# Kernel optimization log

Hardware: AMD Instinct MI355X
Metric: run time of the kernel (lower is better)

Reference implementation:

```python
import jax, jax.numpy as jnp
import numpy as np

E = 1024
H = 16
D = E // H  # 64
SCALE = float(D ** 0.5)  # module MULTIPLIES by sqrt(d_head), faithful to source


def setup_inputs() -> dict:
    key = jax.random.key(0)
    k1, k2, k3 = jax.random.split(key, 3)
    x = jax.random.normal(k1, (4, 2048, E), dtype=jnp.float32)
    # store weights as [in, out] so forward is x @ W (equiv to torch Linear with W.T)
    w_qkv = jax.random.normal(k2, (E, 3 * E), dtype=jnp.float32) * (1.0 / np.sqrt(E))
    w_out = jax.random.normal(k3, (E, E), dtype=jnp.float32) * (1.0 / np.sqrt(E))
    return {"x": x, "w_qkv": w_qkv, "w_out": w_out}


def reference(x, w_qkv, w_out):
    b, t, _ = x.shape
    qkv = x @ w_qkv  # [b, t, 3E]
    # einops 'b t (d k h) -> k b h t d' with k=3, h=H: innermost axis is h
    qkv = qkv.reshape(b, t, D, 3, H)
    qkv = jnp.transpose(qkv, (3, 0, 4, 1, 2))  # [3, b, h, t, d]
    q, k, v = qkv[0], qkv[1], qkv[2]
    energy = jnp.einsum('bhid,bhjd->bhij', q, k) * SCALE  # note: multiply, per source
    attn = jax.nn.softmax(energy, axis=-1)
    o = jnp.einsum('bhij,bhjd->bhid', attn, v)
    o = jnp.transpose(o, (0, 2, 1, 3)).reshape(b, t, H * D)  # 'b h t d -> b t (h d)'
    return o @ w_out
```

## Files before the change

### kernel.cpp

```cpp
#include <hip/hip_runtime.h>

typedef __attribute__((ext_vector_type(4))) float f32x4;
typedef __attribute__((ext_vector_type(16))) float f32x16;
typedef __attribute__((ext_vector_type(8))) short bf16x8;
typedef __attribute__((ext_vector_type(4))) unsigned short u16x4;

#define NB 4
#define NT 2048
#define NE 1024
#define NH 16
#define ND 64
#define NM (NB*NT)

__device__ inline unsigned short f2bf(float f){
  unsigned int u = __float_as_uint(f);
  return (unsigned short)((u + 0x7fffu + ((u >> 16) & 1u)) >> 16);
}
__device__ inline float bf2f(unsigned short s){
  return __uint_as_float(((unsigned int)s) << 16);
}
__device__ inline unsigned short f2h(float f){
  union { _Float16 h; unsigned short u; } c;
  c.h = (_Float16)f;
  return c.u;
}
__device__ inline float h2f(unsigned short s){
  union { _Float16 h; unsigned short u; } c;
  c.u = s;
  return (float)c.h;
}
__device__ inline f32x4 mfma16b(bf16x8 a, bf16x8 b, f32x4 c){
  return __builtin_amdgcn_mfma_f32_16x16x32_bf16(a, b, c, 0, 0, 0);
}
__device__ inline f32x4 mfma16h(bf16x8 a, bf16x8 b, f32x4 c){
  return __builtin_amdgcn_mfma_f32_16x16x32_f16(a, b, c, 0, 0, 0);
}
__device__ inline f32x16 mfma32h(bf16x8 a, bf16x8 b, f32x16 c){
  return __builtin_amdgcn_mfma_f32_32x32x16_f16(a, b, c, 0, 0, 0);
}
__device__ inline void gload_lds16(const unsigned short* g, unsigned short* l){
  __builtin_amdgcn_global_load_lds(
      (const __attribute__((address_space(1))) void*)g,
      (__attribute__((address_space(3))) void*)l, 16, 0, 0);
}
__device__ inline float max3f(float a, float b, float c){
  float r;
  asm("v_max3_f32 %0, %1, %2, %3" : "=v"(r) : "v"(a), "v"(b), "v"(c));
  return r;
}

__global__ __launch_bounds__(256) void prep_x_k(const float* __restrict__ x,
    unsigned short* __restrict__ xh, int n4){
  int stride = gridDim.x * 256;
  for (int i = blockIdx.x * 256 + threadIdx.x; i < n4; i += stride){
    f32x4 v = ((const f32x4*)x)[i];
    u16x4 o;
    #pragma unroll
    for (int j = 0; j < 4; j++) o[j] = f2h(v[j]);
    ((u16x4*)xh)[i] = o;
  }
}

__global__ __launch_bounds__(256) void prep_wq_k(const float* __restrict__ w,
    unsigned short* __restrict__ wq){
  __shared__ float tile[32][33];
  int tx = threadIdx.x & 31, ty = threadIdx.x >> 5;
  int c0 = blockIdx.x * 32, k0 = blockIdx.y * 32;
  #pragma unroll
  for (int i = 0; i < 32; i += 8)
    tile[ty + i][tx] = w[(size_t)(k0 + ty + i) * 3072 + c0 + tx];
  __syncthreads();
  #pragma unroll
  for (int i = 0; i < 32; i += 8){
    int col = c0 + ty + i;
    int d = col / 48, r = col % 48;
    int kk = r >> 4, h = r & 15;
    int n = kk * 1024 + h * 64 + d;
    wq[(size_t)n * NE + k0 + tx] = f2h(tile[tx][ty + i]);
  }
}

__global__ __launch_bounds__(256) void prep_wo_k(const float* __restrict__ w,
    unsigned short* __restrict__ wt){
  __shared__ float tile[32][33];
  int tx = threadIdx.x & 31, ty = threadIdx.x >> 5;
  int n0 = blockIdx.x * 32, k0 = blockIdx.y * 32;
  #pragma unroll
  for (int i = 0; i < 32; i += 8)
    tile[ty + i][tx] = w[(size_t)(k0 + ty + i) * NE + n0 + tx];
  __syncthreads();
  #pragma unroll
  for (int i = 0; i < 32; i += 8)
    wt[(size_t)(n0 + ty + i) * NE + k0 + tx] = f2bf(tile[tx][ty + i]);
}

template<int EPI>
__global__ __launch_bounds__(256) void gemm_k(
    const unsigned short* __restrict__ A,
    const unsigned short* __restrict__ Bt,
    float* __restrict__ Cf,
    unsigned short* __restrict__ Qh,
    unsigned short* __restrict__ Kh, unsigned short* __restrict__ Kl,
    unsigned short* __restrict__ Vt,
    int M, int N, int K){
  __shared__ unsigned short lds[2][128 * 32];
  const int tid = threadIdx.x;
  const int w = tid >> 6, l = tid & 63;
  const int wr = w >> 1, wc = w & 1;
  const int m0 = blockIdx.y * 128, n0 = blockIdx.x * 128;

  f32x4 acc[4][4];
  #pragma unroll
  for (int i = 0; i < 4; i++)
    #pragma unroll
    for (int j = 0; j < 4; j++) acc[i][j] = (f32x4){0.f, 0.f, 0.f, 0.f};

  const int lr = l >> 2;
  const int lkb = (l & 3) * 8;

  for (int k0 = 0; k0 < K; k0 += 32){
    #pragma unroll
    for (int cc = 0; cc < 2; cc++){
      int c = w + cc * 4;
      gload_lds16(A  + (size_t)(m0 + c * 16 + lr) * K + k0 + lkb, &lds[0][c * 512]);
      gload_lds16(Bt + (size_t)(n0 + c * 16 + lr) * K + k0 + lkb, &lds[1][c * 512]);
    }
    __syncthreads();
    bf16x8 af[4], bfr[4];
    #pragma unroll
    for (int mi = 0; mi < 4; mi++)
      af[mi] = *(bf16x8*)&lds[0][(wr * 64 + mi * 16 + (l & 15)) * 32 + (l >> 4) * 8];
    #pragma unroll
    for (int ni = 0; ni < 4; ni++)
      bfr[ni] = *(bf16x8*)&lds[1][(wc * 64 + ni * 16 + (l & 15)) * 32 + (l >> 4) * 8];
    #pragma unroll
    for (int mi = 0; mi < 4; mi++)
      #pragma unroll
      for (int ni = 0; ni < 4; ni++)
        acc[mi][ni] = EPI ? mfma16h(af[mi], bfr[ni], acc[mi][ni])
                          : mfma16b(af[mi], bfr[ni], acc[mi][ni]);
    __syncthreads();
  }

  #pragma unroll
  for (int mi = 0; mi < 4; mi++){
    #pragma unroll
    for (int ni = 0; ni < 4; ni++){
      #pragma unroll
      for (int j = 0; j < 4; j++){
        int row = m0 + wr * 64 + mi * 16 + (l >> 4) * 4 + j;
        int col = n0 + wc * 64 + ni * 16 + (l & 15);
        float v = acc[mi][ni][j];
        if (EPI == 0){
          Cf[(size_t)row * N + col] = v;
        } else {
          int kk = col >> 10, h = (col >> 6) & 15, d = col & 63;
          int bb = row >> 11, t = row & (NT - 1);
          if (kk == 2){
            Vt[((size_t)(bb * NH + h) * ND + d) * NT + t] = f2h(v);
          } else {
            size_t off = ((size_t)(bb * NH + h) * NT + t) * ND + d;
            if (kk == 0){
              Qh[off] = f2h(v);
            } else {
              unsigned short hi = f2h(v);
              Kh[off] = hi; Kl[off] = f2h(v - h2f(hi));
            }
          }
        }
      }
    }
  }
}

__global__ __launch_bounds__(256, 3) void attn_k(
    const unsigned short* __restrict__ Qh,
    const unsigned short* __restrict__ Kh, const unsigned short* __restrict__ Kl,
    const unsigned short* __restrict__ Vt, unsigned short* __restrict__ O){
  __shared__ unsigned short kh_lds[2][64 * 64];
  __shared__ unsigned short kl_lds[2][64 * 64];
  __shared__ unsigned short vt_lds[2][64 * 64];
  const int tid = threadIdx.x;
  const int w = tid >> 6, l = tid & 63;
  const int qi = l & 31, hi = l >> 5;
  const int bid = blockIdx.x;
  const int xcd = bid & 7, slot = bid >> 3;
  const int bh_i = xcd + 8 * (slot >> 4);
  const int qt = slot & 15;
  const int b = bh_i >> 4, h = bh_i & 15;
  const int i0 = qt * 128 + w * 32;
  const size_t bh = (size_t)bh_i;

  const unsigned short* KhG = Kh + bh * NT * ND;
  const unsigned short* KlG = Kl + bh * NT * ND;
  const unsigned short* VtG = Vt + bh * ND * NT;

  bf16x8 qh[4];
  {
    const unsigned short* qb = Qh + (bh * NT + i0 + qi) * ND + hi * 8;
    #pragma unroll
    for (int c = 0; c < 4; c++) qh[c] = *(const bf16x8*)(qb + c * 16);
  }

  f32x16 o0, o1;
  #pragma unroll
  for (int r = 0; r < 16; r++){ o0[r] = 0.f; o1[r] = 0.f; }
  float mrun = -3.0e38f, lrun = 0.f;

  const int rk = l >> 3;
  const int ck = (l & 7) ^ rk;

  auto STAGE = [&](int buf, int j0){
    gload_lds16(KhG + (size_t)(j0 + 16 * w + rk) * ND + ck * 8,     &kh_lds[buf][(16 * w) * 64]);
    gload_lds16(KhG + (size_t)(j0 + 16 * w + 8 + rk) * ND + ck * 8, &kh_lds[buf][(16 * w + 8) * 64]);
    gload_lds16(KlG + (size_t)(j0 + 16 * w + rk) * ND + ck * 8,     &kl_lds[buf][(16 * w) * 64]);
    gload_lds16(KlG + (size_t)(j0 + 16 * w + 8 + rk) * ND + ck * 8, &kl_lds[buf][(16 * w + 8) * 64]);
    gload_lds16(VtG + (size_t)(16 * w + rk) * NT + j0 + ck * 8,     &vt_lds[buf][(16 * w) * 64]);
    gload_lds16(VtG + (size_t)(16 * w + 8 + rk) * NT + j0 + ck * 8, &vt_lds[buf][(16 * w + 8) * 64]);
  };

  auto STEP = [&](int buf, int half){
    const char* KH = (const char*)&kh_lds[buf][0];
    const char* KL = (const char*)&kl_lds[buf][0];
    const char* VT = (const char*)&vt_lds[buf][0];
    bf16x8 kh[4], kl[4];
    #pragma unroll
    for (int c = 0; c < 4; c++){
      int off = (half * 32 + qi) * 128 + (((2 * c + hi) ^ (qi & 7)) * 16);
      kh[c] = *(const bf16x8*)(KH + off);
      kl[c] = *(const bf16x8*)(KL + off);
    }

    f32x16 t1, t2;
    #pragma unroll
    for (int r = 0; r < 16; r++){ t1[r] = 0.f; t2[r] = 0.f; }
    __builtin_amdgcn_s_setprio(1);
    #pragma unroll
    for (int c = 0; c < 4; c++){
      t1 = mfma32h(kh[c], qh[c], t1);
      t2 = mfma32h(kl[c], qh[c], t2);
    }
    __builtin_amdgcn_s_setprio(0);
    f32x16 s = t1 + t2;

    bf16x8 vb[2][2];
    #pragma unroll
    for (int dt = 0; dt < 2; dt++)
      #pragma unroll
      for (int k0 = 0; k0 < 2; k0++){
        int off = (dt * 32 + qi) * 128 + (((half * 4 + 2 * k0 + hi) ^ (qi & 7)) * 16);
        vb[dt][k0] = *(const bf16x8*)(VT + off);
      }

    float m1 = max3f(s[0], s[1], s[2]);
    float m2 = max3f(s[3], s[4], s[5]);
    float m3 = max3f(s[6], s[7], s[8]);
    float m4 = max3f(s[9], s[10], s[11]);
    float m5 = max3f(s[12], s[13], s[14]);
    float pm = fmaxf(max3f(m1, m2, m3), max3f(m4, m5, s[15]));
    pm = fmaxf(pm, __shfl_xor(pm, 32));
    float Lm = pm * 8.0f;
    if (!__all(Lm <= mrun + 8.0f)){
      float nm = fmaxf(mrun, Lm);
      float sc = __expf(mrun - nm);
      mrun = nm;
      lrun *= sc;
      #pragma unroll
      for (int r = 0; r < 16; r++){
        int mrow = (r & 3) + 8 * (r >> 2) + 4 * hi;
        float scr = __shfl(sc, mrow);
        o0[r] *= scr;
        o1[r] *= scr;
      }
    }
    float p[16];
    #pragma unroll
    for (int r = 0; r < 16; r++) p[r] = __expf(fmaf(s[r], 8.0f, -mrun));
    float u8[8], u4[4];
    #pragma unroll
    for (int i = 0; i < 8; i++) u8[i] = p[2 * i] + p[2 * i + 1];
    #pragma unroll
    for (int i = 0; i < 4; i++) u4[i] = u8[2 * i] + u8[2 * i + 1];
    float rs = (u4[0] + u4[1]) + (u4[2] + u4[3]);
    rs += __shfl_xor(rs, 32);
    lrun += rs;

    unsigned int pk[8];
    #pragma unroll
    for (int i = 0; i < 8; i++)
      asm("v_cvt_pkrtz_f16_f32 %0, %1, %2" : "=v"(pk[i]) : "v"(p[2 * i]), "v"(p[2 * i + 1]));
    unsigned int sw[8];
    #pragma unroll
    for (int i = 0; i < 8; i++) sw[i] = __shfl_xor(pk[i], 32);

    union { unsigned int u[4]; bf16x8 v; } pa0, pa1;
    pa0.u[0] = hi ? sw[2] : pk[0];
    pa0.u[1] = hi ? sw[3] : pk[1];
    pa0.u[2] = hi ? pk[2] : sw[0];
    pa0.u[3] = hi ? pk[3] : sw[1];
    pa1.u[0] = hi ? sw[6] : pk[4];
    pa1.u[1] = hi ? sw[7] : pk[5];
    pa1.u[2] = hi ? pk[6] : sw[4];
    pa1.u[3] = hi ? pk[7] : sw[5];

    __builtin_amdgcn_s_setprio(1);
    o0 = mfma32h(pa0.v, vb[0][0], o0);
    o0 = mfma32h(pa1.v, vb[0][1], o0);
    o1 = mfma32h(pa0.v, vb[1][0], o1);
    o1 = mfma32h(pa1.v, vb[1][1], o1);
    __builtin_amdgcn_s_setprio(0);
  };

  STAGE(0, 0);
  asm volatile("s_waitcnt vmcnt(0)" ::: "memory");
  __syncthreads();
  int buf = 0;
  for (int j0 = 0; j0 < NT; j0 += 64){
    if (j0 + 64 < NT) STAGE(buf ^ 1, j0 + 64);
    STEP(buf, 0);
    STEP(buf, 1);
    __syncthreads();
    buf ^= 1;
  }

  float rl = 1.0f / lrun;
  #pragma unroll
  for (int r = 0; r < 16; r++){
    int mrow = (r & 3) + 8 * (r >> 2) + 4 * hi;
    float f = __shfl(rl, mrow);
    size_t base = ((size_t)b * NT + i0 + mrow) * NE + h * ND + qi;
    O[base]      = f2bf(o0[r] * f);
    O[base + 32] = f2bf(o1[r] * f);
  }
}

extern "C" void kernel_launch(void* const* d_in, const int* in_sizes, int n_in,
                              void* d_out, int out_size, void* d_ws, size_t ws_size,
                              hipStream_t stream){
  const float* x     = (const float*)d_in[0];
  const float* w_qkv = (const float*)d_in[1];
  const float* w_out = (const float*)d_in[2];
  float* out = (float*)d_out;

  char* ws = (char*)d_ws;
  const size_t SZ_X  = (size_t)NM * NE * 2;
  const size_t SZ_WQ = (size_t)3072 * NE * 2;
  const size_t SZ_WO = (size_t)NE * NE * 2;
  const size_t SZ_T  = (size_t)NB * NH * NT * ND * 2;

  unsigned short* xh  = (unsigned short*)(ws);
  unsigned short* wq  = (unsigned short*)(ws + SZ_X);
  unsigned short* wto = (unsigned short*)(ws + SZ_X + SZ_WQ);
  unsigned short* Qh  = (unsigned short*)(ws + SZ_X + SZ_WQ + SZ_WO);
  unsigned short* Kh  = Qh + (SZ_T / 2);
  unsigned short* Kl  = Qh + 2 * (SZ_T / 2);
  unsigned short* Vt  = Qh + 3 * (SZ_T / 2);
  unsigned short* Obuf = xh;

  const size_t NEED = SZ_X + SZ_WQ + SZ_WO + 4 * SZ_T;
  if (ws_size < NEED) return;

  prep_x_k<<<2048, 256, 0, stream>>>(x, xh, NM * NE / 4);
  prep_wq_k<<<dim3(3072 / 32, 1024 / 32), 256, 0, stream>>>(w_qkv, wq);
  prep_wo_k<<<dim3(1024 / 32, 1024 / 32), 256, 0, stream>>>(w_out, wto);
  gemm_k<1><<<dim3(3072 / 128, NM / 128), 256, 0, stream>>>(
      xh, wq, nullptr, Qh, Kh, Kl, Vt, NM, 3072, NE);
  attn_k<<<dim3(1024), 256, 0, stream>>>(Qh, Kh, Kl, Vt, Obuf);
  gemm_k<0><<<dim3(NE / 128, NM / 128), 256, 0, stream>>>(
      Obuf, wto, out, nullptr, nullptr, nullptr, nullptr, NM, NE, NE);
}
```

Measured before the change: 304.5 us.

## Process two query tiles per attention block to reuse staged K/V tiles

Each attention workgroup now handles 256 query rows (two independent 128-row tiles, A and B) instead of 128, running the online-softmax step twice over each staged K/V tile. The grid halves to 512 blocks and the launch-bounds occupancy hint drops from 3 to 2. This halves global-to-LDS traffic for K and V per query row and the sync overhead per unit of work. In exchange it doubles accumulator and Q register usage and leaves fewer blocks to fill the GPU.

```diff
diff --git a/kernel.cpp b/kernel.cpp
--- a/kernel.cpp
+++ b/kernel.cpp
@@ -173,7 +173,7 @@
   }
 }
 
-__global__ __launch_bounds__(256, 3) void attn_k(
+__global__ __launch_bounds__(256, 2) void attn_k(
     const unsigned short* __restrict__ Qh,
     const unsigned short* __restrict__ Kh, const unsigned short* __restrict__ Kl,
     const unsigned short* __restrict__ Vt, unsigned short* __restrict__ O){
@@ -185,27 +185,33 @@
   const int qi = l & 31, hi = l >> 5;
   const int bid = blockIdx.x;
   const int xcd = bid & 7, slot = bid >> 3;
-  const int bh_i = xcd + 8 * (slot >> 4);
-  const int qt = slot & 15;
+  const int bh_i = xcd + 8 * (slot >> 3);
+  const int qt = slot & 7;
   const int b = bh_i >> 4, h = bh_i & 15;
-  const int i0 = qt * 128 + w * 32;
+  const int i0A = qt * 256 + w * 32;
+  const int i0B = i0A + 128;
   const size_t bh = (size_t)bh_i;
 
   const unsigned short* KhG = Kh + bh * NT * ND;
   const unsigned short* KlG = Kl + bh * NT * ND;
   const unsigned short* VtG = Vt + bh * ND * NT;
 
-  bf16x8 qh[4];
+  bf16x8 qhA[4], qhB[4];
   {
-    const unsigned short* qb = Qh + (bh * NT + i0 + qi) * ND + hi * 8;
-    #pragma unroll
-    for (int c = 0; c < 4; c++) qh[c] = *(const bf16x8*)(qb + c * 16);
-  }
-
-  f32x16 o0, o1;
-  #pragma unroll
-  for (int r = 0; r < 16; r++){ o0[r] = 0.f; o1[r] = 0.f; }
-  float mrun = -3.0e38f, lrun = 0.f;
+    const unsigned short* qa = Qh + (bh * NT + i0A + qi) * ND + hi * 8;
+    const unsigned short* qb = Qh + (bh * NT + i0B + qi) * ND + hi * 8;
+    #pragma unroll
+    for (int c = 0; c < 4; c++){
+      qhA[c] = *(const bf16x8*)(qa + c * 16);
+      qhB[c] = *(const bf16x8*)(qb + c * 16);
+    }
+  }
+
+  f32x16 oA0, oA1, oB0, oB1;
+  #pragma unroll
+  for (int r = 0; r < 16; r++){ oA0[r] = 0.f; oA1[r] = 0.f; oB0[r] = 0.f; oB1[r] = 0.f; }
+  float mrunA = -3.0e38f, lrunA = 0.f;
+  float mrunB = -3.0e38f, lrunB = 0.f;
 
   const int rk = l >> 3;
   const int ck = (l & 7) ^ rk;
@@ -219,7 +225,8 @@
     gload_lds16(VtG + (size_t)(16 * w + 8 + rk) * NT + j0 + ck * 8, &vt_lds[buf][(16 * w + 8) * 64]);
   };
 
-  auto STEP = [&](int buf, int half){
+  auto STEP = [&](int buf, int half, const bf16x8 (&qh)[4],
+                  f32x16& o0, f32x16& o1, float& mrun, float& lrun){
     const char* KH = (const char*)&kh_lds[buf][0];
     const char* KL = (const char*)&kl_lds[buf][0];
     const char* VT = (const char*)&vt_lds[buf][0];
@@ -317,20 +324,27 @@
   int buf = 0;
   for (int j0 = 0; j0 < NT; j0 += 64){
     if (j0 + 64 < NT) STAGE(buf ^ 1, j0 + 64);
-    STEP(buf, 0);
-    STEP(buf, 1);
+    STEP(buf, 0, qhA, oA0, oA1, mrunA, lrunA);
+    STEP(buf, 1, qhA, oA0, oA1, mrunA, lrunA);
+    STEP(buf, 0, qhB, oB0, oB1, mrunB, lrunB);
+    STEP(buf, 1, qhB, oB0, oB1, mrunB, lrunB);
     __syncthreads();
     buf ^= 1;
   }
 
-  float rl = 1.0f / lrun;
+  float rlA = 1.0f / lrunA;
+  float rlB = 1.0f / lrunB;
   #pragma unroll
   for (int r = 0; r < 16; r++){
     int mrow = (r & 3) + 8 * (r >> 2) + 4 * hi;
-    float f = __shfl(rl, mrow);
-    size_t base = ((size_t)b * NT + i0 + mrow) * NE + h * ND + qi;
-    O[base]      = f2bf(o0[r] * f);
-    O[base + 32] = f2bf(o1[r] * f);
+    float fA = __shfl(rlA, mrow);
+    float fB = __shfl(rlB, mrow);
+    size_t baseA = ((size_t)b * NT + i0A + mrow) * NE + h * ND + qi;
+    size_t baseB = ((size_t)b * NT + i0B + mrow) * NE + h * ND + qi;
+    O[baseA]      = f2bf(oA0[r] * fA);
+    O[baseA + 32] = f2bf(oA1[r] * fA);
+    O[baseB]      = f2bf(oB0[r] * fB);
+    O[baseB + 32] = f2bf(oB1[r] * fB);
   }
 }
 
@@ -365,7 +379,7 @@
   prep_wo_k<<<dim3(1024 / 32, 1024 / 32), 256, 0, stream>>>(w_out, wto);
   gemm_k<1><<<dim3(3072 / 128, NM / 128), 256, 0, stream>>>(
       xh, wq, nullptr, Qh, Kh, Kl, Vt, NM, 3072, NE);
-  attn_k<<<dim3(1024), 256, 0, stream>>>(Qh, Kh, Kl, Vt, Obuf);
+  attn_k<<<dim3(512), 256, 0, stream>>>(Qh, Kh, Kl, Vt, Obuf);
   gemm_k<0><<<dim3(NE / 128, NM / 128), 256, 0, stream>>>(
       Obuf, wto, out, nullptr, nullptr, nullptr, nullptr, NM, NE, NE);
 }
```

Result: faster. 295.6 us, median of 2 (-2.9%).
